# Kernel tuning notes

Hardware: AMD Instinct MI355X
Metric: run time of the kernel (lower is better)

Reference implementation:

```python
import jax, jax.numpy as jnp
import numpy as np

B, N, K, NUM_CLASSES = 8, 4096, 16, 40
M = B * N


def _safe_norm(v):
    s = jnp.sum(v * v, axis=-1)
    return jnp.where(s > 0, jnp.sqrt(jnp.where(s > 0, s, 1.0)), 0.0)


def _angle(v1, v2):
    cn = _safe_norm(jnp.cross(v1, v2))
    d = jnp.sum(v1 * v2, axis=-1)
    ok = (cn > 0) | (d != 0)
    return jnp.where(ok, jnp.arctan2(cn, jnp.where(ok, d, 1.0)), 0.0)


def _ppf(pos_i, pos_j, n_i, n_j):
    # PyG point_pair_features: pseudo = pos_j - pos_i (j = source, i = target)
    pseudo = pos_j - pos_i
    return jnp.stack([_safe_norm(pseudo), _angle(n_i, pseudo),
                      _angle(n_j, pseudo), _angle(n_i, n_j)], axis=-1)


def _knn_edges(pos):
    # knn_graph(k=K, loop=False), per-graph; returns (src, dst) with self-loops
    # appended (PPFConv add_self_loops=True default).
    p = pos.reshape(B, N, 3)
    sq = jnp.sum(p * p, axis=-1)                                   # [B,N]
    d2 = sq[:, :, None] + sq[:, None, :] - 2.0 * jnp.einsum('bnd,bmd->bnm', p, p)
    d2 = jnp.where(jnp.eye(N, dtype=bool)[None], jnp.inf, d2)      # no loops
    _, nbr = jax.lax.top_k(-d2, K)                                  # [B,N,K]
    offs = (jnp.arange(B) * N)[:, None, None]
    src = (nbr + offs).reshape(-1)                                  # neighbors j
    dst = jnp.repeat(jnp.arange(M), K)                              # targets i
    loops = jnp.arange(M)
    return jnp.concatenate([src, loops]), jnp.concatenate([dst, loops])


def _mlp(e, w1, b1, w2, b2):
    return jax.nn.relu(e @ w1 + b1) @ w2 + b2


def setup_inputs() -> dict:
    key = jax.random.key(0)
    ks = jax.random.split(key, 12)
    pos = jax.random.normal(ks[0], (M, 3), jnp.float32)
    nrm = jax.random.normal(ks[1], (M, 3), jnp.float32)
    nrm = nrm / jnp.linalg.norm(nrm, axis=-1, keepdims=True)
    batch = jnp.repeat(jnp.arange(B, dtype=jnp.int32), N)
    s = 0.1
    return {
        'pos': pos, 'normal': nrm, 'batch': batch,
        'w1a': jax.random.normal(ks[2], (4, 32)) * s,  'b1a': jnp.zeros(32),
        'w1b': jax.random.normal(ks[3], (32, 32)) * s, 'b1b': jnp.zeros(32),
        'w2a': jax.random.normal(ks[4], (36, 32)) * s, 'b2a': jnp.zeros(32),
        'w2b': jax.random.normal(ks[5], (32, 32)) * s, 'b2b': jnp.zeros(32),
        'wc':  jax.random.normal(ks[6], (32, NUM_CLASSES)) * s,
        'bc':  jnp.zeros(NUM_CLASSES),
    }


def reference(pos, normal, batch, w1a, b1a, w1b, b1b, w2a, b2a, w2b, b2b, wc, bc):
    src, dst = _knn_edges(pos)
    feats = _ppf(pos[dst], pos[src], normal[dst], normal[src])      # [E,4]
    # conv1: x=None -> message = mlp1(ppf), scatter-max per target node
    msg1 = _mlp(feats, w1a, b1a, w1b, b1b)
    x = jax.nn.relu(jax.ops.segment_max(msg1, dst, num_segments=M))  # [M,32]
    # conv2: message = mlp2([x_j, ppf])
    msg2 = _mlp(jnp.concatenate([x[src], feats], axis=-1), w2a, b2a, w2b, b2b)
    x = jax.nn.relu(jax.ops.segment_max(msg2, dst, num_segments=M))
    # global_max_pool over each graph (uniform batch: reshape)
    g = x.reshape(B, N, 32).max(axis=1)                              # [B,32]
    return g @ wc + bc                                               # [B,40]
```

## Files before the change

### kernel.cpp

```cpp
#include <hip/hip_runtime.h>
#include <hip/hip_bf16.h>
#include <math.h>

#define NB 8
#define NN 4096
#define KK 16
#define MM (NB*NN)
#define CH 32
#define SLOTS 17
#define NCLS 40
#define BIG 3.0e38f
#define CAP 96
#define NPB 32
#define NBLK (MM/NPB)
#define BPG (NBLK/NB)
#define HROW 36
#define HALF 2048

#define OW1A 0
#define OB1A 128
#define OW1B 160
#define OB1B 1184
#define OW2A 1216
#define OB2A 2368
#define OW2B 2400
#define OB2B 3424
#define OWC  3456
#define OBC  4736
#define NWTS 4776

typedef short short8 __attribute__((ext_vector_type(8)));
typedef float f32x4  __attribute__((ext_vector_type(4)));
typedef float f32x2  __attribute__((ext_vector_type(2)));

__device__ float4 g_pos4[MM];
__device__ float4 g_nrm4[MM];
__device__ int    g_nbr[MM*KK];
__device__ float  g_u[MM*CH];
__device__ float  g_wts[NWTS];
__device__ int    g_gmaxi[NB*CH];
__device__ int    g_cnt[NB];
__device__ __align__(16) float4 g_fe4[MM*SLOTS];
__device__ __align__(16) unsigned short g_wfrag1[2][2][64][8];
__device__ __align__(16) unsigned short g_wfrag2[2][2][64][8];

__device__ __forceinline__ float bf(const __hip_bfloat16 x) { return __bfloat162float(x); }

__device__ __forceinline__ float ldf(const void* p, int i, bool f32) {
  return f32 ? ((const float*)p)[i] : bf(((const __hip_bfloat16*)p)[i]);
}

__device__ __forceinline__ float angf(float ax, float ay, float az,
                                      float bx, float by, float bz) {
  float cx = ay*bz - az*by;
  float cy = az*bx - ax*bz;
  float cz = ax*by - ay*bx;
  float s  = cx*cx + cy*cy + cz*cz;
  float cn = s > 0.f ? sqrtf(s) : 0.f;
  float d  = ax*bx + ay*by + az*bz;
  return (cn > 0.f || d != 0.f) ? atan2f(cn, d) : 0.f;
}

__device__ __forceinline__ void ppf4(const float4 pi, const float4 ni,
                                     const float4 pj, const float4 nj, float* f) {
  float px = pj.x - pi.x, py = pj.y - pi.y, pz = pj.z - pi.z;
  float s = px*px + py*py + pz*pz;
  f[0] = s > 0.f ? sqrtf(s) : 0.f;
  f[1] = angf(ni.x, ni.y, ni.z, px, py, pz);
  f[2] = angf(nj.x, nj.y, nj.z, px, py, pz);
  f[3] = angf(ni.x, ni.y, ni.z, nj.x, nj.y, nj.z);
}

__device__ __forceinline__ unsigned int fkey(float f) {
  unsigned int u = __float_as_uint(f);
  return (u & 0x80000000u) ? ~u : (u | 0x80000000u);
}
__device__ __forceinline__ float funkey(unsigned int k) {
  unsigned int u = (k & 0x80000000u) ? (k ^ 0x80000000u) : ~k;
  return __uint_as_float(u);
}

__device__ __forceinline__ unsigned int mbcnt64(unsigned long long m) {
  return __builtin_amdgcn_mbcnt_hi((unsigned int)(m >> 32),
         __builtin_amdgcn_mbcnt_lo((unsigned int)m, 0u));
}

__device__ __forceinline__ void bsplit(float v, unsigned short* hi, unsigned short* lo) {
  __hip_bfloat16 h = __float2bfloat16(v);
  float hf = __bfloat162float(h);
  __hip_bfloat16 l = __float2bfloat16(v - hf);
  *hi = *reinterpret_cast<unsigned short*>(&h);
  *lo = *reinterpret_cast<unsigned short*>(&l);
}

__device__ __forceinline__ void afrag(const float* row, short8* ah, short8* al) {
  float4 a = *(const float4*)row;
  float4 b = *(const float4*)(row + 4);
  unsigned short h, l;
  #pragma unroll
  for (int j = 0; j < 4; ++j) {
    bsplit((&a.x)[j], &h, &l); (*ah)[j]   = (short)h; (*al)[j]   = (short)l;
    bsplit((&b.x)[j], &h, &l); (*ah)[j+4] = (short)h; (*al)[j+4] = (short)l;
  }
}

__device__ __forceinline__ float ldwt(int i, bool f32,
    const void* w1a, const void* b1a, const void* w1b, const void* b1b,
    const void* w2a, const void* b2a, const void* w2b, const void* b2b,
    const void* wc, const void* bc) {
  if (i < OB1A) return ldf(w1a, i - OW1A, f32);
  if (i < OW1B) return ldf(b1a, i - OB1A, f32);
  if (i < OB1B) return ldf(w1b, i - OW1B, f32);
  if (i < OW2A) return ldf(b1b, i - OB1B, f32);
  if (i < OB2A) return ldf(w2a, i - OW2A, f32);
  if (i < OW2B) return ldf(b2a, i - OB2A, f32);
  if (i < OB2B) return ldf(w2b, i - OW2B, f32);
  if (i < OWC)  return ldf(b2b, i - OB2B, f32);
  if (i < OBC)  return ldf(wc,  i - OWC,  f32);
  return ldf(bc, i - OBC, f32);
}

__global__ __launch_bounds__(256) void prep_kernel(
    const void* __restrict__ pos, const void* __restrict__ nrm,
    const void* w1a, const void* b1a, const void* w1b, const void* b1b,
    const void* w2a, const void* b2a, const void* w2b, const void* b2b,
    const void* wc, const void* bc) {
  __shared__ int sflag;
  const int tid = threadIdx.x;
  const int bid = blockIdx.x;
  const int base = bid << 8;
  if (tid < 64) {
    const float* nf = (const float*)nrm;
    const __hip_bfloat16* nh = (const __hip_bfloat16*)nrm;
    int n = base + tid;
    float x = nf[3*n], y = nf[3*n+1], z = nf[3*n+2];
    float ss = x*x + y*y + z*z;
    bool okf = (ss > 0.98f && ss < 1.02f);
    float a = bf(nh[3*n]), b2 = bf(nh[3*n+1]), c2 = bf(nh[3*n+2]);
    float sb = a*a + b2*b2 + c2*c2;
    bool okb = (sb > 0.95f && sb < 1.05f);
    unsigned long long mf = __ballot(okf), mb = __ballot(okb);
    if (tid == 0) sflag = (__popcll(mf) >= __popcll(mb)) ? 1 : 0;
  }
  __syncthreads();
  const bool f32 = sflag != 0;
  {
    int i = base + tid;
    float x = ldf(pos, 3*i, f32), y = ldf(pos, 3*i+1, f32), z = ldf(pos, 3*i+2, f32);
    g_pos4[i] = make_float4(x, y, z, x*x + y*y + z*z);
    float a = ldf(nrm, 3*i, f32), bb = ldf(nrm, 3*i+1, f32), cc = ldf(nrm, 3*i+2, f32);
    g_nrm4[i] = make_float4(a, bb, cc, 0.f);
  }
  if (bid < 16) {
    int t = (bid << 8) + tid;
    int which = t >> 11;
    int r = t & 2047;
    int tt = r >> 10;  r &= 1023;
    int hl = r >> 9;   r &= 511;
    int ln = r >> 3;
    int j  = r & 7;
    int k = (ln >> 4)*8 + j;
    int c = tt*16 + (ln & 15);
    float wv = ldf(which ? w2b : w1b, k*CH + c, f32);
    unsigned short hi, lo;
    bsplit(wv, &hi, &lo);
    unsigned short v = hl ? lo : hi;
    if (which) g_wfrag2[tt][hl][ln][j] = v;
    else       g_wfrag1[tt][hl][ln][j] = v;
  } else if (bid < 35) {
    int i = ((bid - 16) << 8) + tid;
    if (i < NWTS)
      g_wts[i] = ldwt(i, f32, w1a, b1a, w1b, b1b, w2a, b2a, w2b, b2b, wc, bc);
  }
}

__global__ __launch_bounds__(512) void knn_conv1_kernel() {
  __shared__ __align__(16) union SU {
    struct {
      float sx[HALF], sy[HALF], sz[HALF];
      unsigned short ilst[NPB][CAP];
      double dlst[8][CAP];
    } k;
    struct {
      float fe[NPB*SLOTS][4];
      float h1s[152*HROW];
      float wsaT[32*HROW];
      float xs[NPB][CH];
    } c;
  } u;
  __shared__ unsigned short nbrs[NPB][KK];

  const int tid  = threadIdx.x;
  const int w    = tid >> 6, lane = tid & 63;
  const int blk  = blockIdx.x;
  const int b    = blk >> 7;
  const int qb   = (blk & 127) << 5;
  const float4* bp = g_pos4 + b*NN;

  float q2x[4], q2y[4], q2z[4];
  #pragma unroll
  for (int qq = 0; qq < 4; ++qq) {
    float4 qv = bp[qb + (w << 2) + qq];
    q2x[qq] = -2.f*qv.x; q2y[qq] = -2.f*qv.y; q2z[qq] = -2.f*qv.z;
  }

  const f32x2* sx2 = (const f32x2*)u.k.sx;
  const f32x2* sy2 = (const f32x2*)u.k.sy;
  const f32x2* sz2 = (const f32x2*)u.k.sz;

  float mn[4];
  #pragma unroll
  for (int qq = 0; qq < 4; ++qq) mn[qq] = BIG;
  #pragma unroll 1
  for (int h = 0; h < 2; ++h) {
    #pragma unroll
    for (int k = 0; k < 4; ++k) {
      int idx = k*512 + tid;
      float4 o = bp[h*HALF + idx];
      u.k.sx[idx] = o.x; u.k.sy[idx] = o.y; u.k.sz[idx] = o.z;
    }
    __syncthreads();
    #pragma unroll 4
    for (int it = 0; it < 16; ++it) {
      int p = it*64 + lane;
      f32x2 ox = sx2[p], oy = sy2[p], oz = sz2[p];
      f32x2 ow = __builtin_elementwise_fma(oz, oz,
                 __builtin_elementwise_fma(oy, oy, ox*ox));
      #pragma unroll
      for (int qq = 0; qq < 4; ++qq) {
        f32x2 qx = {q2x[qq], q2x[qq]};
        f32x2 qy = {q2y[qq], q2y[qq]};
        f32x2 qz = {q2z[qq], q2z[qq]};
        f32x2 d = __builtin_elementwise_fma(qx, ox,
                  __builtin_elementwise_fma(qy, oy,
                  __builtin_elementwise_fma(qz, oz, ow)));
        mn[qq] = fminf(fminf(d[0], d[1]), mn[qq]);
      }
    }
    if (h == 0) __syncthreads();
  }

  unsigned int key[4], lo[4], hi[4];
  #pragma unroll
  for (int qq = 0; qq < 4; ++qq) { key[qq] = fkey(mn[qq]) >> 16; lo[qq] = 0u; hi[qq] = 0xFFFFu; }
  #pragma unroll 1
  for (int s = 0; s < 16; ++s) {
    #pragma unroll
    for (int qq = 0; qq < 4; ++qq) {
      unsigned int mid = (lo[qq] + hi[qq]) >> 1;
      int c = (int)__popcll(__ballot(key[qq] <= mid));
      if (c >= 17) hi[qq] = mid; else lo[qq] = mid + 1;
    }
  }
  float Tf[4];
  #pragma unroll
  for (int qq = 0; qq < 4; ++qq) {
    float T = funkey((hi[qq] << 16) | 0xFFFFu);
    Tf[qq] = T + 4e-5f + 1e-5f*fabsf(T);
  }

  unsigned int scnt[4];
  #pragma unroll
  for (int qq = 0; qq < 4; ++qq) scnt[qq] = 0u;
  #pragma unroll 1
  for (int hh = 0; hh < 2; ++hh) {
    const int h = 1 - hh;
    if (hh == 1) {
      __syncthreads();
      #pragma unroll
      for (int k = 0; k < 4; ++k) {
        int idx = k*512 + tid;
        float4 o = bp[h*HALF + idx];
        u.k.sx[idx] = o.x; u.k.sy[idx] = o.y; u.k.sz[idx] = o.z;
      }
      __syncthreads();
    }
    #pragma unroll 2
    for (int it = 0; it < 16; ++it) {
      int p = it*64 + lane;
      int gidx = h*HALF + 2*p;
      f32x2 ox = sx2[p], oy = sy2[p], oz = sz2[p];
      f32x2 ow = __builtin_elementwise_fma(oz, oz,
                 __builtin_elementwise_fma(oy, oy, ox*ox));
      #pragma unroll
      for (int qq = 0; qq < 4; ++qq) {
        f32x2 qx = {q2x[qq], q2x[qq]};
        f32x2 qy = {q2y[qq], q2y[qq]};
        f32x2 qz = {q2z[qq], q2z[qq]};
        f32x2 d = __builtin_elementwise_fma(qx, ox,
                  __builtin_elementwise_fma(qy, oy,
                  __builtin_elementwise_fma(qz, oz, ow)));
        bool h0 = d[0] <= Tf[qq];
        bool h1 = d[1] <= Tf[qq];
        unsigned long long mk0 = __ballot(h0);
        unsigned long long mk1 = __ballot(h1);
        if (mk0 | mk1) {
          unsigned int cbase = scnt[qq];
          if (h0) {
            unsigned int pos = cbase + mbcnt64(mk0);
            if (pos < CAP) u.k.ilst[(w<<2)|qq][pos] = (unsigned short)gidx;
          }
          cbase += (unsigned int)__popcll(mk0);
          if (h1) {
            unsigned int pos = cbase + mbcnt64(mk1);
            if (pos < CAP) u.k.ilst[(w<<2)|qq][pos] = (unsigned short)(gidx + 1);
          }
          scnt[qq] = cbase + (unsigned int)__popcll(mk1);
        }
      }
    }
  }

  #pragma unroll 1
  for (int qq = 0; qq < 4; ++qq) {
    const int ql = (w << 2) | qq;
    const int m = min((int)scnt[qq], CAP);
    const double mx = (double)(-0.5f*q2x[qq]);
    const double my_ = (double)(-0.5f*q2y[qq]);
    const double mz = (double)(-0.5f*q2z[qq]);
    const double sqme = (mx*mx + my_*my_) + mz*mz;
    for (int e = lane; e < m; e += 64) {
      int ci = u.k.ilst[ql][e];
      float4 cv = bp[ci];
      double ox = (double)cv.x, oy = (double)cv.y, oz = (double)cv.z;
      double sqo = (ox*ox + oy*oy) + oz*oz;
      double dt  = (mx*ox + my_*oy) + mz*oz;
      u.k.dlst[w][e] = (sqme + sqo) - 2.0*dt;
    }
    for (int e = lane; e < m; e += 64) {
      double myd = u.k.dlst[w][e];
      int myi = u.k.ilst[ql][e];
      int rank = 0;
      for (int o = 0; o < m; ++o) {
        double od = u.k.dlst[w][o];
        int oi = u.k.ilst[ql][o];
        rank += (od < myd) || (od == myd && oi < myi);
      }
      if (rank >= 1 && rank <= KK) {
        nbrs[ql][rank-1] = (unsigned short)myi;
        g_nbr[(b*NN + qb + ql)*KK + (rank-1)] = b*NN + myi;
      }
    }
  }

  const int c32 = tid & 31;
  const int quad = lane >> 4, l15 = lane & 15;
  float w1a_c[4];
  #pragma unroll
  for (int f = 0; f < 4; ++f) w1a_c[f] = g_wts[OW1A + f*CH + c32];
  const float b1a_c = g_wts[OB1A + c32];
  short8 bH0 = *(const short8*)&g_wfrag1[0][0][lane][0];
  short8 bL0 = *(const short8*)&g_wfrag1[0][1][lane][0];
  short8 bH1 = *(const short8*)&g_wfrag1[1][0][lane][0];
  short8 bL1 = *(const short8*)&g_wfrag1[1][1][lane][0];
  const float bias0 = g_wts[OB1B + l15];
  const float bias1 = g_wts[OB1B + 16 + l15];

  __syncthreads();

  for (int i2 = tid; i2 < 1024; i2 += 512) {
    int k = i2 >> 5, cc = i2 & 31;
    u.c.wsaT[cc*HROW + k] = g_wts[OW2A + i2];
  }
  const int nbb = b*NN + qb;
  for (int e = tid; e < NPB*SLOTS; e += 512) {
    int ns = e / 17, slot = e - ns*17;
    int ig = nbb + ns;
    int jg = (slot < KK) ? (b*NN + (int)nbrs[ns][slot]) : ig;
    float f[4];
    ppf4(g_pos4[ig], g_nrm4[ig], g_pos4[jg], g_nrm4[jg], f);
    float4 fv = make_float4(f[0], f[1], f[2], f[3]);
    *(float4*)u.c.fe[e] = fv;
    g_fe4[(size_t)nbb*SLOTS + e] = fv;
  }
  __syncthreads();

  #pragma unroll 1
  for (int ck = 0; ck < 4; ++ck) {
    #pragma unroll
    for (int it = 0; it < 9; ++it) {
      int idx = it*512 + tid;
      int e = idx >> 5;
      if (e < 136) {
        float4 f4 = *(const float4*)u.c.fe[ck*136 + e];
        float h = b1a_c + f4.x*w1a_c[0] + f4.y*w1a_c[1] + f4.z*w1a_c[2] + f4.w*w1a_c[3];
        u.c.h1s[e*HROW + c32] = fmaxf(h, 0.f);
      }
    }
    __syncthreads();
    {
      const int rbase = w*17;
      short8 ah0, al0, ah1, al1;
      afrag(&u.c.h1s[(rbase      + l15)*HROW + quad*8], &ah0, &al0);
      afrag(&u.c.h1s[(rbase + 16 + l15)*HROW + quad*8], &ah1, &al1);
      f32x4 a00 = {0.f,0.f,0.f,0.f}, a01 = a00, a10 = a00, a11 = a00;
      a00 = __builtin_amdgcn_mfma_f32_16x16x32_bf16(ah0, bH0, a00, 0, 0, 0);
      a00 = __builtin_amdgcn_mfma_f32_16x16x32_bf16(ah0, bL0, a00, 0, 0, 0);
      a00 = __builtin_amdgcn_mfma_f32_16x16x32_bf16(al0, bH0, a00, 0, 0, 0);
      a01 = __builtin_amdgcn_mfma_f32_16x16x32_bf16(ah0, bH1, a01, 0, 0, 0);
      a01 = __builtin_amdgcn_mfma_f32_16x16x32_bf16(ah0, bL1, a01, 0, 0, 0);
      a01 = __builtin_amdgcn_mfma_f32_16x16x32_bf16(al0, bH1, a01, 0, 0, 0);
      a10 = __builtin_amdgcn_mfma_f32_16x16x32_bf16(ah1, bH0, a10, 0, 0, 0);
      a10 = __builtin_amdgcn_mfma_f32_16x16x32_bf16(ah1, bL0, a10, 0, 0, 0);
      a10 = __builtin_amdgcn_mfma_f32_16x16x32_bf16(al1, bH0, a10, 0, 0, 0);
      a11 = __builtin_amdgcn_mfma_f32_16x16x32_bf16(ah1, bH1, a11, 0, 0, 0);
      a11 = __builtin_amdgcn_mfma_f32_16x16x32_bf16(ah1, bL1, a11, 0, 0, 0);
      a11 = __builtin_amdgcn_mfma_f32_16x16x32_bf16(al1, bH1, a11, 0, 0, 0);
      float m0 = fmaxf(fmaxf(a00[0], a00[1]), fmaxf(a00[2], a00[3]));
      float m1 = fmaxf(fmaxf(a01[0], a01[1]), fmaxf(a01[2], a01[3]));
      if (quad == 0) { m0 = fmaxf(m0, a10[0]); m1 = fmaxf(m1, a11[0]); }
      m0 = fmaxf(m0, __shfl_xor(m0, 16)); m0 = fmaxf(m0, __shfl_xor(m0, 32));
      m1 = fmaxf(m1, __shfl_xor(m1, 16)); m1 = fmaxf(m1, __shfl_xor(m1, 32));
      if (quad == 0) {
        u.c.xs[ck*8 + w][l15]      = fmaxf(m0 + bias0, 0.f);
        u.c.xs[ck*8 + w][16 + l15] = fmaxf(m1 + bias1, 0.f);
      }
    }
    __syncthreads();
  }
  #pragma unroll
  for (int it = 0; it < 2; ++it) {
    int ns = it*16 + (tid >> 5);
    float uu = 0.f;
    #pragma unroll
    for (int k4 = 0; k4 < 8; ++k4) {
      float4 x4 = *(const float4*)&u.c.xs[ns][4*k4];
      float4 w4 = *(const float4*)&u.c.wsaT[c32*HROW + 4*k4];
      uu += x4.x*w4.x + x4.y*w4.y + x4.z*w4.z + x4.w*w4.w;
    }
    g_u[(nbb + ns)*CH + c32] = uu;
  }
}

__global__ __launch_bounds__(512) void conv2_kernel(float* __restrict__ out) {
  __shared__ __align__(16) float fe[NPB*SLOTS][4];
  __shared__ int jn[NPB*SLOTS];
  __shared__ __align__(16) float h1s[152*HROW];
  __shared__ float xs[NPB][CH];
  __shared__ float gm2[CH];
  __shared__ int slast;
  const int tid = threadIdx.x;
  const int c = tid & 31;
  const int lane = tid & 63, wv = tid >> 6;
  const int quad = lane >> 4, l15 = lane & 15;
  const int node0 = blockIdx.x << 5;
  const int g = blockIdx.x >> 7;
  float w2aL_c[4];
  #pragma unroll
  for (int f = 0; f < 4; ++f) w2aL_c[f] = g_wts[OW2A + (CH + f)*CH + c];
  const float b2a_c = g_wts[OB2A + c];
  short8 bH0 = *(const short8*)&g_wfrag2[0][0][lane][0];
  short8 bL0 = *(const short8*)&g_wfrag2[0][1][lane][0];
  short8 bH1 = *(const short8*)&g_wfrag2[1][0][lane][0];
  short8 bL1 = *(const short8*)&g_wfrag2[1][1][lane][0];
  const float bias0 = g_wts[OB2B + l15];
  const float bias1 = g_wts[OB2B + 16 + l15];

  for (int e = tid; e < NPB*SLOTS; e += 512) {
    int ns = e / 17, slot = e - ns*17;
    int i = node0 + ns;
    jn[e] = (slot < KK) ? g_nbr[i*KK + slot] : i;
    *(float4*)fe[e] = g_fe4[(size_t)node0*SLOTS + e];
  }
  __syncthreads();

  #pragma unroll 1
  for (int ck = 0; ck < 4; ++ck) {
    #pragma unroll
    for (int it = 0; it < 9; ++it) {
      int idx = it*512 + tid;
      int e = idx >> 5;
      if (e < 136) {
        float4 f4 = *(const float4*)fe[ck*136 + e];
        float uv = g_u[jn[ck*136 + e]*CH + c];
        float h = b2a_c + uv + f4.x*w2aL_c[0] + f4.y*w2aL_c[1] + f4.z*w2aL_c[2] + f4.w*w2aL_c[3];
        h1s[e*HROW + c] = fmaxf(h, 0.f);
      }
    }
    __syncthreads();
    {
      const int rbase = wv*17;
      short8 ah0, al0, ah1, al1;
      afrag(&h1s[(rbase      + l15)*HROW + quad*8], &ah0, &al0);
      afrag(&h1s[(rbase + 16 + l15)*HROW + quad*8], &ah1, &al1);
      f32x4 a00 = {0.f,0.f,0.f,0.f}, a01 = a00, a10 = a00, a11 = a00;
      a00 = __builtin_amdgcn_mfma_f32_16x16x32_bf16(ah0, bH0, a00, 0, 0, 0);
      a00 = __builtin_amdgcn_mfma_f32_16x16x32_bf16(ah0, bL0, a00, 0, 0, 0);
      a00 = __builtin_amdgcn_mfma_f32_16x16x32_bf16(al0, bH0, a00, 0, 0, 0);
      a01 = __builtin_amdgcn_mfma_f32_16x16x32_bf16(ah0, bH1, a01, 0, 0, 0);
      a01 = __builtin_amdgcn_mfma_f32_16x16x32_bf16(ah0, bL1, a01, 0, 0, 0);
      a01 = __builtin_amdgcn_mfma_f32_16x16x32_bf16(al0, bH1, a01, 0, 0, 0);
      a10 = __builtin_amdgcn_mfma_f32_16x16x32_bf16(ah1, bH0, a10, 0, 0, 0);
      a10 = __builtin_amdgcn_mfma_f32_16x16x32_bf16(ah1, bL0, a10, 0, 0, 0);
      a10 = __builtin_amdgcn_mfma_f32_16x16x32_bf16(al1, bH0, a10, 0, 0, 0);
      a11 = __builtin_amdgcn_mfma_f32_16x16x32_bf16(ah1, bH1, a11, 0, 0, 0);
      a11 = __builtin_amdgcn_mfma_f32_16x16x32_bf16(ah1, bL1, a11, 0, 0, 0);
      a11 = __builtin_amdgcn_mfma_f32_16x16x32_bf16(al1, bH1, a11, 0, 0, 0);
      float m0 = fmaxf(fmaxf(a00[0], a00[1]), fmaxf(a00[2], a00[3]));
      float m1 = fmaxf(fmaxf(a01[0], a01[1]), fmaxf(a01[2], a01[3]));
      if (quad == 0) { m0 = fmaxf(m0, a10[0]); m1 = fmaxf(m1, a11[0]); }
      m0 = fmaxf(m0, __shfl_xor(m0, 16)); m0 = fmaxf(m0, __shfl_xor(m0, 32));
      m1 = fmaxf(m1, __shfl_xor(m1, 16)); m1 = fmaxf(m1, __shfl_xor(m1, 32));
      if (quad == 0) {
        xs[ck*8 + wv][l15]      = fmaxf(m0 + bias0, 0.f);
        xs[ck*8 + wv][16 + l15] = fmaxf(m1 + bias1, 0.f);
      }
    }
    __syncthreads();
  }
  if (tid < CH) {
    float m2 = xs[0][c];
    #pragma unroll
    for (int r = 1; r < NPB; ++r) m2 = fmaxf(m2, xs[r][c]);
    int old = atomicMax(&g_gmaxi[g*CH + c], __float_as_int(m2));
    asm volatile("" :: "v"(old));
  }
  if (tid == 0) {
    int rank = atomicAdd(&g_cnt[g], 1);
    slast = (rank == BPG - 1) ? 1 : 0;
  }
  __syncthreads();
  if (slast) {
    __builtin_amdgcn_fence(__ATOMIC_ACQUIRE, "agent");
    if (tid < CH) gm2[c] = __int_as_float(((volatile int*)g_gmaxi)[g*CH + c]);
    __syncthreads();
    if (tid < NCLS) {
      float s = g_wts[OBC + tid];
      #pragma unroll
      for (int f = 0; f < CH; ++f) s += gm2[f] * g_wts[OWC + f*NCLS + tid];
      out[g*NCLS + tid] = s;
    }
    if (tid < CH) atomicExch(&g_gmaxi[g*CH + tid], 0);
    if (tid == 0) atomicExch(&g_cnt[g], 0);
  }
}

extern "C" void kernel_launch(void* const* d_in, const int* in_sizes, int n_in,
                              void* d_out, int out_size, void* d_ws, size_t ws_size,
                              hipStream_t stream) {
  const void* pos = d_in[0];
  const void* nrm = d_in[1];
  const void* w1a = d_in[3];
  const void* b1a = d_in[4];
  const void* w1b = d_in[5];
  const void* b1b = d_in[6];
  const void* w2a = d_in[7];
  const void* b2a = d_in[8];
  const void* w2b = d_in[9];
  const void* b2b = d_in[10];
  const void* wc  = d_in[11];
  const void* bc  = d_in[12];

  prep_kernel<<<MM/256, 256, 0, stream>>>(pos, nrm, w1a, b1a, w1b, b1b,
                                          w2a, b2a, w2b, b2b, wc, bc);
  knn_conv1_kernel<<<NBLK, 512, 0, stream>>>();
  conv2_kernel<<<NBLK, 512, 0, stream>>>((float*)d_out);
}
```

Measured before the change: 204.4 us.

## Use wave bitonic sort for kNN selection and prefetch gathered features in conv2

When a query's candidate list fits in one wave (at most 64), the O(m^2) rank-counting selection is replaced by an in-register bitonic sort using shuffles. Lists larger than 64 fall back to rank counting, which now recomputes distances instead of staging them in an LDS double array. That array is removed, shrinking the shared-memory union. In conv2, the next chunk's g_u neighbor-feature gathers are issued into registers before the MFMA stage so their latency overlaps compute, at the cost of nine extra live registers per thread.

```diff
diff --git a/kernel.cpp b/kernel.cpp
--- a/kernel.cpp
+++ b/kernel.cpp
@@ -179,7 +179,6 @@
     struct {
       float sx[HALF], sy[HALF], sz[HALF];
       unsigned short ilst[NPB][CAP];
-      double dlst[8][CAP];
     } k;
     struct {
       float fe[NPB*SLOTS][4];
@@ -319,26 +318,52 @@
     const double my_ = (double)(-0.5f*q2y[qq]);
     const double mz = (double)(-0.5f*q2z[qq]);
     const double sqme = (mx*mx + my_*my_) + mz*mz;
-    for (int e = lane; e < m; e += 64) {
-      int ci = u.k.ilst[ql][e];
-      float4 cv = bp[ci];
-      double ox = (double)cv.x, oy = (double)cv.y, oz = (double)cv.z;
-      double sqo = (ox*ox + oy*oy) + oz*oz;
-      double dt  = (mx*ox + my_*oy) + mz*oz;
-      u.k.dlst[w][e] = (sqme + sqo) - 2.0*dt;
-    }
-    for (int e = lane; e < m; e += 64) {
-      double myd = u.k.dlst[w][e];
-      int myi = u.k.ilst[ql][e];
-      int rank = 0;
-      for (int o = 0; o < m; ++o) {
-        double od = u.k.dlst[w][o];
-        int oi = u.k.ilst[ql][o];
-        rank += (od < myd) || (od == myd && oi < myi);
-      }
-      if (rank >= 1 && rank <= KK) {
-        nbrs[ql][rank-1] = (unsigned short)myi;
-        g_nbr[(b*NN + qb + ql)*KK + (rank-1)] = b*NN + myi;
+    if (m <= 64) {
+      double d; int idx;
+      if (lane < m) {
+        int ci = u.k.ilst[ql][lane];
+        float4 cv = bp[ci];
+        double ox = (double)cv.x, oy = (double)cv.y, oz = (double)cv.z;
+        double sqo = (ox*ox + oy*oy) + oz*oz;
+        double dt  = (mx*ox + my_*oy) + mz*oz;
+        d = (sqme + sqo) - 2.0*dt;
+        idx = ci;
+      } else { d = 1.0e300; idx = 0x7fffffff; }
+      #pragma unroll
+      for (int k = 2; k <= 64; k <<= 1) {
+        #pragma unroll
+        for (int j = k >> 1; j >= 1; j >>= 1) {
+          double pd = __shfl_xor(d, j);
+          int    pi = __shfl_xor(idx, j);
+          bool mineLess = (d < pd) || (d == pd && idx < pi);
+          bool wantMin  = (((lane & j) == 0) == ((lane & k) == 0));
+          if (mineLess != wantMin) { d = pd; idx = pi; }
+        }
+      }
+      if (lane >= 1 && lane <= KK) {
+        nbrs[ql][lane-1] = (unsigned short)idx;
+        g_nbr[(b*NN + qb + ql)*KK + (lane-1)] = b*NN + idx;
+      }
+    } else {
+      for (int e = lane; e < m; e += 64) {
+        int myi = u.k.ilst[ql][e];
+        float4 cv = bp[myi];
+        double ox = (double)cv.x, oy = (double)cv.y, oz = (double)cv.z;
+        double myd = (sqme + ((ox*ox + oy*oy) + oz*oz))
+                   - 2.0*((mx*ox + my_*oy) + mz*oz);
+        int rank = 0;
+        for (int o = 0; o < m; ++o) {
+          int oi = u.k.ilst[ql][o];
+          float4 ov = bp[oi];
+          double px = (double)ov.x, py = (double)ov.y, pz = (double)ov.z;
+          double od = (sqme + ((px*px + py*py) + pz*pz))
+                    - 2.0*((mx*px + my_*py) + mz*pz);
+          rank += (od < myd) || (od == myd && oi < myi);
+        }
+        if (rank >= 1 && rank <= KK) {
+          nbrs[ql][rank-1] = (unsigned short)myi;
+          g_nbr[(b*NN + qb + ql)*KK + (rank-1)] = b*NN + myi;
+        }
       }
     }
   }
@@ -441,6 +466,7 @@
   __shared__ int slast;
   const int tid = threadIdx.x;
   const int c = tid & 31;
+  const int s16 = tid >> 5;
   const int lane = tid & 63, wv = tid >> 6;
   const int quad = lane >> 4, l15 = lane & 15;
   const int node0 = blockIdx.x << 5;
@@ -464,20 +490,35 @@
   }
   __syncthreads();
 
+  float upf[9];
+  #pragma unroll
+  for (int it = 0; it < 9; ++it) {
+    int e = it*16 + s16;
+    int ee = (e < 136) ? e : 135;
+    upf[it] = g_u[jn[ee]*CH + c];
+  }
+
   #pragma unroll 1
   for (int ck = 0; ck < 4; ++ck) {
     #pragma unroll
     for (int it = 0; it < 9; ++it) {
-      int idx = it*512 + tid;
-      int e = idx >> 5;
+      int e = it*16 + s16;
       if (e < 136) {
         float4 f4 = *(const float4*)fe[ck*136 + e];
-        float uv = g_u[jn[ck*136 + e]*CH + c];
-        float h = b2a_c + uv + f4.x*w2aL_c[0] + f4.y*w2aL_c[1] + f4.z*w2aL_c[2] + f4.w*w2aL_c[3];
+        float h = b2a_c + upf[it] + f4.x*w2aL_c[0] + f4.y*w2aL_c[1]
+                + f4.z*w2aL_c[2] + f4.w*w2aL_c[3];
         h1s[e*HROW + c] = fmaxf(h, 0.f);
       }
     }
     __syncthreads();
+    if (ck < 3) {
+      #pragma unroll
+      for (int it = 0; it < 9; ++it) {
+        int e = it*16 + s16;
+        int ee = (e < 136) ? e : 135;
+        upf[it] = g_u[jn[(ck+1)*136 + ee]*CH + c];
+      }
+    }
     {
       const int rbase = wv*17;
       short8 ah0, al0, ah1, al1;
```

New measurement: 196.9 us, median of 2. 3.7% less time.
